# Optimization experiments

Hardware: AMD Instinct MI355X
Metric: run time of the kernel (lower is better)

## Reference

```python
import jax, jax.numpy as jnp
import numpy as np

B = 64            # batch of graphs
E = 8978          # edge-simplices per graph (nodes of the Hodge-1 graph)
E2 = E // 2       # after Graclus pair-pooling
K = 4             # Laguerre polynomial order
DEG = 16          # avg degree of the (edge-)adjacency
SLOPE = 0.33      # LeakyReLU negative slope
EPS = 1e-5        # BatchNorm eps


def _make_edges(rng, b, n, deg):
    # block-diagonal batched edge list: each graph only connects within itself
    offs = np.repeat(np.arange(b, dtype=np.int64) * n, n * deg)
    dst = np.tile(np.repeat(np.arange(n, dtype=np.int64), deg), b) + offs
    src = rng.integers(0, n, size=b * n * deg) + offs
    return np.stack([src, dst]).astype(np.int32)


def setup_inputs() -> dict:
    rng = np.random.default_rng(0)
    ks = jax.random.split(jax.random.key(0), 12)
    N1 = B * E
    ei1 = _make_edges(rng, B, E, DEG)
    ei2 = _make_edges(rng, B, E2, DEG)
    return {
        "x_s": jax.random.normal(ks[0], (N1, 1), jnp.float32),
        "edge_index_s": jnp.asarray(ei1),
        "edge_weight_s": jax.random.uniform(ks[1], (ei1.shape[1],), jnp.float32) * (2.0 / DEG),
        "edge_index_s1": jnp.asarray(ei2),
        "edge_weight_s1": jax.random.uniform(ks[2], (ei2.shape[1],), jnp.float32) * (2.0 / DEG),
        "W0": jax.random.normal(ks[3], (K, 1, 32), jnp.float32) * 0.3,
        "b0": jnp.zeros((32,), jnp.float32),
        "g0": jnp.ones((32,), jnp.float32),
        "be0": jnp.zeros((32,), jnp.float32),
        "W1": jax.random.normal(ks[4], (K, 32, 32), jnp.float32) * 0.1,
        "b1": jnp.zeros((32,), jnp.float32),
        "g1": jnp.ones((32,), jnp.float32),
        "be1": jnp.zeros((32,), jnp.float32),
        "W2": jax.random.normal(ks[5], (K, 32, 1), jnp.float32) * 0.1,
        "b2": jnp.zeros((1,), jnp.float32),
        "g2": jnp.ones((1,), jnp.float32),
        "be2": jnp.zeros((1,), jnp.float32),
        "lin1_W": jax.random.normal(ks[6], (E2, 256), jnp.float32) * 0.02,
        "lin1_b": jnp.zeros((256,), jnp.float32),
        "bn1_g": jnp.ones((256,), jnp.float32),
        "bn1_b": jnp.zeros((256,), jnp.float32),
        "lin2_W": jax.random.normal(ks[7], (256, 128), jnp.float32) * 0.06,
        "lin2_b": jnp.zeros((128,), jnp.float32),
        "bn2_g": jnp.ones((128,), jnp.float32),
        "bn2_b": jnp.zeros((128,), jnp.float32),
        "lin3_W": jax.random.normal(ks[8], (128, 1), jnp.float32) * 0.09,
        "lin3_b": jnp.zeros((1,), jnp.float32),
    }


def _laguerre_layer(x, src, dst, ew, W, b, gamma, beta, n):
    """HodgeLaguerreConv (K-order Laguerre recurrence over sparse L) + BatchNorm + LeakyReLU."""
    def matvec(v):  # (L v)[i] = sum_j w_ij v[j]
        return jax.ops.segment_sum(ew[:, None] * v[src], dst, num_segments=n)
    Tp = x                      # L_0(L) x = x
    out = Tp @ W[0]
    Tc = x - matvec(x)          # L_1(L) x = x - L x
    out = out + Tc @ W[1]
    for k in range(1, K - 1):   # L_{k+1} = ((2k+1-L) L_k - k L_{k-1}) / (k+1)
        Tn = ((2 * k + 1) * Tc - matvec(Tc) - k * Tp) / (k + 1)
        out = out + Tn @ W[k + 1]
        Tp, Tc = Tc, Tn
    out = out + b
    out = gamma * (out - out.mean(0)) * jax.lax.rsqrt(out.var(0) + EPS) + beta
    return jnp.where(out > 0, out, SLOPE * out)


def _bn(h, g, b):
    return g * (h - h.mean(0)) * jax.lax.rsqrt(h.var(0) + EPS) + b


def reference(x_s, edge_index_s, edge_weight_s, edge_index_s1, edge_weight_s1,
              W0, b0, g0, be0, W1, b1, g1, be1, W2, b2, g2, be2,
              lin1_W, lin1_b, bn1_g, bn1_b, lin2_W, lin2_b, bn2_g, bn2_b,
              lin3_W, lin3_b):
    N1, N2 = B * E, B * E2
    x = _laguerre_layer(x_s, edge_index_s[0], edge_index_s[1], edge_weight_s,
                        W0, b0, g0, be0, N1)
    # Graclus pooling: merge matched node pairs by max over features
    x = x.reshape(B, E2, 2, x.shape[-1]).max(axis=2).reshape(N2, -1)
    x = _laguerre_layer(x, edge_index_s1[0], edge_index_s1[1], edge_weight_s1,
                        W1, b1, g1, be1, N2)
    x = _laguerre_layer(x, edge_index_s1[0], edge_index_s1[1], edge_weight_s1,
                        W2, b2, g2, be2, N2)
    x = x.reshape(B, E2)        # last conv has 1 channel
    h = jax.nn.relu(_bn(x @ lin1_W + lin1_b, bn1_g, bn1_b))
    h = jax.nn.relu(_bn(h @ lin2_W + lin2_b, bn2_g, bn2_b))
    return h @ lin3_W + lin3_b  # [B, num_classes=1]
```

## Files before the change

### kernel.cpp

```cpp
#include <hip/hip_runtime.h>
#include <cstdint>

#define SLOPE 0.33f

static constexpr int B_   = 64;
static constexpr int E1_  = 8978;
static constexpr int E2_  = 4489;
static constexpr int N1_  = B_ * E1_;
static constexpr int N2_  = B_ * E2_;
static constexpr int DEG_ = 16;
static constexpr int QTR_ = 2245;
static constexpr int QTR2_ = 1123;
static constexpr int MVGRID = (N2_ * 32) / 256;
static constexpr int PROJ_GRID = (N2_ + 511) / 512;
static constexpr double EPS_ = 1e-5;

__device__ __forceinline__ float lrelu(float v) { return v > 0.f ? v : SLOPE * v; }
__device__ __forceinline__ float dot4(float4 a, float4 b) {
  return a.x * b.x + a.y * b.y + a.z * b.z + a.w * b.w;
}

__global__ __launch_bounds__(256) void k0_mv1(const float* __restrict__ x,
    const int* __restrict__ src, const float* __restrict__ ew, float* __restrict__ T1) {
  __shared__ float sx[E1_];
  int g = blockIdx.x >> 2, q = blockIdx.x & 3;
  int gbase = g * E1_;
  for (int j = threadIdx.x; j < E1_; j += 256) sx[j] = x[gbase + j];
  __syncthreads();
  int start = q * QTR_, end = min(start + QTR_, E1_);
  for (int i = start + (int)threadIdx.x; i < end; i += 256) {
    int node = gbase + i;
    const int4* s4 = (const int4*)(src + (size_t)node * DEG_);
    const float4* w4 = (const float4*)(ew + (size_t)node * DEG_);
    float acc = 0.f;
#pragma unroll
    for (int j = 0; j < 4; ++j) {
      int4 s = s4[j]; float4 w = w4[j];
      acc += w.x * sx[s.x - gbase] + w.y * sx[s.y - gbase]
           + w.z * sx[s.z - gbase] + w.w * sx[s.w - gbase];
    }
    T1[node] = sx[i] - acc;
  }
}

__global__ __launch_bounds__(256) void k0_mv2(const float* __restrict__ x,
    const int* __restrict__ src, const float* __restrict__ ew,
    const float* __restrict__ T1, float* __restrict__ T2) {
  __shared__ float sT[E1_];
  int g = blockIdx.x >> 2, q = blockIdx.x & 3;
  int gbase = g * E1_;
  for (int j = threadIdx.x; j < E1_; j += 256) sT[j] = T1[gbase + j];
  __syncthreads();
  int start = q * QTR_, end = min(start + QTR_, E1_);
  for (int i = start + (int)threadIdx.x; i < end; i += 256) {
    int node = gbase + i;
    const int4* s4 = (const int4*)(src + (size_t)node * DEG_);
    const float4* w4 = (const float4*)(ew + (size_t)node * DEG_);
    float acc = 0.f;
#pragma unroll
    for (int j = 0; j < 4; ++j) {
      int4 s = s4[j]; float4 w = w4[j];
      acc += w.x * sT[s.x - gbase] + w.y * sT[s.y - gbase]
           + w.z * sT[s.z - gbase] + w.w * sT[s.w - gbase];
    }
    T2[node] = (3.f * sT[i] - acc - x[node]) * 0.5f;
  }
}

__global__ __launch_bounds__(256) void k0_mv3(const float* __restrict__ x,
    const int* __restrict__ src, const float* __restrict__ ew,
    const float* __restrict__ T1, const float* __restrict__ T2,
    float* __restrict__ T3, double* mom) {
  __shared__ float sT[E1_];
  __shared__ double sred[4 * 14];
  int g = blockIdx.x >> 2, q = blockIdx.x & 3;
  int gbase = g * E1_;
  for (int j = threadIdx.x; j < E1_; j += 256) sT[j] = T2[gbase + j];
  __syncthreads();
  double m[14];
#pragma unroll
  for (int j = 0; j < 14; ++j) m[j] = 0.0;
  int start = q * QTR_, end = min(start + QTR_, E1_);
  for (int i = start + (int)threadIdx.x; i < end; i += 256) {
    int node = gbase + i;
    const int4* s4 = (const int4*)(src + (size_t)node * DEG_);
    const float4* w4 = (const float4*)(ew + (size_t)node * DEG_);
    float acc = 0.f;
#pragma unroll
    for (int j = 0; j < 4; ++j) {
      int4 s = s4[j]; float4 w = w4[j];
      acc += w.x * sT[s.x - gbase] + w.y * sT[s.y - gbase]
           + w.z * sT[s.z - gbase] + w.w * sT[s.w - gbase];
    }
    float t1 = T1[node];
    float t2 = sT[i];
    float t3 = (5.f * t2 - acc - 2.f * t1) * (1.f / 3.f);
    T3[node] = t3;
    double d0 = x[node], d1 = t1, d2 = t2, d3 = t3;
    m[0] += d0; m[1] += d1; m[2] += d2; m[3] += d3;
    m[4] += d0 * d0; m[5] += d0 * d1; m[6] += d0 * d2; m[7] += d0 * d3;
    m[8] += d1 * d1; m[9] += d1 * d2; m[10] += d1 * d3;
    m[11] += d2 * d2; m[12] += d2 * d3; m[13] += d3 * d3;
  }
  int lane = threadIdx.x & 63, wid = threadIdx.x >> 6;
#pragma unroll
  for (int j = 0; j < 14; ++j) {
    double v = m[j];
    for (int o = 32; o; o >>= 1) v += __shfl_down(v, o);
    if (lane == 0) sred[wid * 14 + j] = v;
  }
  __syncthreads();
  if (threadIdx.x < 14) {
    double s = sred[threadIdx.x] + sred[14 + threadIdx.x] + sred[28 + threadIdx.x] + sred[42 + threadIdx.x];
    atomicAdd(&mom[threadIdx.x], s);
  }
}

__global__ void k0_params(const double* __restrict__ mom, const float* __restrict__ W0,
    const float* __restrict__ g0, const float* __restrict__ be0,
    float* __restrict__ scale0, float* __restrict__ shiftE0) {
  int c = threadIdx.x;
  if (c >= 32) return;
  double inv = 1.0 / (double)N1_;
  double mm[4];
#pragma unroll
  for (int k = 0; k < 4; ++k) mm[k] = mom[k] * inv;
  double M[4][4];
  M[0][0] = mom[4] * inv;  M[0][1] = mom[5] * inv;  M[0][2] = mom[6] * inv;  M[0][3] = mom[7] * inv;
  M[1][1] = mom[8] * inv;  M[1][2] = mom[9] * inv;  M[1][3] = mom[10] * inv;
  M[2][2] = mom[11] * inv; M[2][3] = mom[12] * inv; M[3][3] = mom[13] * inv;
  M[1][0] = M[0][1]; M[2][0] = M[0][2]; M[3][0] = M[0][3];
  M[2][1] = M[1][2]; M[3][1] = M[1][3]; M[3][2] = M[2][3];
  double w[4];
#pragma unroll
  for (int k = 0; k < 4; ++k) w[k] = W0[k * 32 + c];
  double mean = 0.0;
#pragma unroll
  for (int k = 0; k < 4; ++k) mean += w[k] * mm[k];
  double e2 = 0.0;
#pragma unroll
  for (int k = 0; k < 4; ++k)
#pragma unroll
    for (int l = 0; l < 4; ++l) e2 += M[k][l] * w[k] * w[l];
  double var = e2 - mean * mean;
  double sc = (double)g0[c] / sqrt(var + EPS_);
  scale0[c] = (float)sc;
  shiftE0[c] = (float)((double)be0[c] - sc * mean);
}

__global__ __launch_bounds__(256) void k0_pool(const float* __restrict__ x,
    const float* __restrict__ T1, const float* __restrict__ T2, const float* __restrict__ T3,
    const float* __restrict__ W0, const float* __restrict__ scale0,
    const float* __restrict__ shiftE0, float* __restrict__ x1) {
  int gid = blockIdx.x * 256 + threadIdx.x;
  int grp = gid >> 5, c = gid & 31;
  if (grp >= N2_) return;
  int b = grp / E2_, j = grp - b * E2_;
  int ga = b * E1_ + 2 * j, gb = ga + 1;
  float w0 = W0[c], w1 = W0[32 + c], w2 = W0[64 + c], w3 = W0[96 + c];
  float da = x[ga] * w0 + T1[ga] * w1 + T2[ga] * w2 + T3[ga] * w3;
  float db = x[gb] * w0 + T1[gb] * w1 + T2[gb] * w2 + T3[gb] * w3;
  float sc = scale0[c], sh = shiftE0[c];
  float ya = lrelu(sc * da + sh), yb = lrelu(sc * db + sh);
  x1[grp * 32 + c] = fmaxf(ya, yb);
}

__global__ __launch_bounds__(256) void k1_projall(const float* __restrict__ X,
    const float* __restrict__ W1, float4* __restrict__ P4) {
  __shared__ float4 Wl[128 * 8];
  const float4 cfs[4] = { {0.f, 0.f, 0.f, -1.f / 6.f},
                          {0.f, 0.f, 0.5f, 1.5f},
                          {0.f, -1.f, -2.f, -3.f},
                          {1.f, 1.f, 1.f, 1.f} };
  for (int e = threadIdx.x; e < 1024; e += 256) {
    int o = e >> 3, qq = e & 7;
    int j = o >> 5, cp = o & 31;
    float4 cf = cfs[j];
    float4 w;
    {
      const float* wp = W1 + (4 * qq + 0) * 32 + cp;
      w.x = cf.x * wp[0] + cf.y * wp[1024] + cf.z * wp[2048] + cf.w * wp[3072];
    }
    {
      const float* wp = W1 + (4 * qq + 1) * 32 + cp;
      w.y = cf.x * wp[0] + cf.y * wp[1024] + cf.z * wp[2048] + cf.w * wp[3072];
    }
    {
      const float* wp = W1 + (4 * qq + 2) * 32 + cp;
      w.z = cf.x * wp[0] + cf.y * wp[1024] + cf.z * wp[2048] + cf.w * wp[3072];
    }
    {
      const float* wp = W1 + (4 * qq + 3) * 32 + cp;
      w.w = cf.x * wp[0] + cf.y * wp[1024] + cf.z * wp[2048] + cf.w * wp[3072];
    }
    Wl[e] = w;
  }
  __syncthreads();
  int rA = blockIdx.x * 512 + threadIdx.x;
  int rB = rA + 256;
  bool okA = rA < N2_, okB = rB < N2_;
  if (!okA) return;
  float4 xA[8], xB[8];
  {
    const float4* pa = (const float4*)(X + (size_t)rA * 32);
#pragma unroll
    for (int t = 0; t < 8; ++t) xA[t] = pa[t];
  }
  if (okB) {
    const float4* pb = (const float4*)(X + (size_t)rB * 32);
#pragma unroll
    for (int t = 0; t < 8; ++t) xB[t] = pb[t];
  } else {
#pragma unroll
    for (int t = 0; t < 8; ++t) xB[t] = {0.f, 0.f, 0.f, 0.f};
  }
  for (int oq = 0; oq < 32; ++oq) {
    float4 aA = {0.f, 0.f, 0.f, 0.f}, aB = {0.f, 0.f, 0.f, 0.f};
    const float4* wr = Wl + oq * 32;
#pragma unroll
    for (int qq = 0; qq < 8; ++qq) {
      float4 w0 = wr[0 * 8 + qq];
      float4 w1 = wr[1 * 8 + qq];
      float4 w2 = wr[2 * 8 + qq];
      float4 w3 = wr[3 * 8 + qq];
      float4 xa = xA[qq], xb = xB[qq];
      aA.x += dot4(xa, w0); aA.y += dot4(xa, w1); aA.z += dot4(xa, w2); aA.w += dot4(xa, w3);
      aB.x += dot4(xb, w0); aB.y += dot4(xb, w1); aB.z += dot4(xb, w2); aB.w += dot4(xb, w3);
    }
    P4[(size_t)oq * N2_ + rA] = aA;
    if (okB) P4[(size_t)oq * N2_ + rB] = aB;
  }
}

__global__ __launch_bounds__(1024) void k1_chain(const float4* __restrict__ P4,
    float4* __restrict__ O4, const int* __restrict__ src,
    const float* __restrict__ ew, double* st) {
  __shared__ float4 bA[E2_], bB[E2_];
  __shared__ float sacc[8];
  int v = (blockIdx.x & 7) * 64 + (blockIdx.x >> 3);
  int g = v >> 3, cg = v & 7;
  int gbase = g * E2_;
  int tid = threadIdx.x;
  if (tid < 8) sacc[tid] = 0.f;
  {
    const float4* sp = P4 + (size_t)cg * N2_ + gbase;
    for (int i = tid; i < E2_; i += 1024) bA[i] = sp[i];
  }
  float4* cur = bA;
  float4* nxt = bB;
  for (int s = 1; s <= 3; ++s) {
    __syncthreads();
    const float4* selfp = P4 + (size_t)(s * 8 + cg) * N2_ + gbase;
    for (int n = tid; n < E2_; n += 1024) {
      const int4* s4 = (const int4*)(src + (size_t)(gbase + n) * DEG_);
      const float4* w4 = (const float4*)(ew + (size_t)(gbase + n) * DEG_);
      float4 acc = selfp[n];
#pragma unroll
      for (int j = 0; j < 4; ++j) {
        int4 sx = s4[j]; float4 w = w4[j];
        float4 g0 = cur[sx.x - gbase];
        float4 g1 = cur[sx.y - gbase];
        float4 g2 = cur[sx.z - gbase];
        float4 g3 = cur[sx.w - gbase];
        acc.x += w.x * g0.x + w.y * g1.x + w.z * g2.x + w.w * g3.x;
        acc.y += w.x * g0.y + w.y * g1.y + w.z * g2.y + w.w * g3.y;
        acc.z += w.x * g0.z + w.y * g1.z + w.z * g2.z + w.w * g3.z;
        acc.w += w.x * g0.w + w.y * g1.w + w.z * g2.w + w.w * g3.w;
      }
      nxt[n] = acc;
    }
    float4* t = cur; cur = nxt; nxt = t;
  }
  __syncthreads();
  float4* op = O4 + (size_t)cg * N2_ + gbase;
  float4 s1 = {0.f, 0.f, 0.f, 0.f}, s2 = {0.f, 0.f, 0.f, 0.f};
  for (int n = tid; n < E2_; n += 1024) {
    float4 vv = cur[n];
    op[n] = vv;
    s1.x += vv.x; s1.y += vv.y; s1.z += vv.z; s1.w += vv.w;
    s2.x += vv.x * vv.x; s2.y += vv.y * vv.y; s2.z += vv.z * vv.z; s2.w += vv.w * vv.w;
  }
  for (int o = 32; o; o >>= 1) {
    s1.x += __shfl_down(s1.x, o); s1.y += __shfl_down(s1.y, o);
    s1.z += __shfl_down(s1.z, o); s1.w += __shfl_down(s1.w, o);
    s2.x += __shfl_down(s2.x, o); s2.y += __shfl_down(s2.y, o);
    s2.z += __shfl_down(s2.z, o); s2.w += __shfl_down(s2.w, o);
  }
  if ((tid & 63) == 0) {
    atomicAdd(&sacc[0], s1.x); atomicAdd(&sacc[1], s1.y);
    atomicAdd(&sacc[2], s1.z); atomicAdd(&sacc[3], s1.w);
    atomicAdd(&sacc[4], s2.x); atomicAdd(&sacc[5], s2.y);
    atomicAdd(&sacc[6], s2.z); atomicAdd(&sacc[7], s2.w);
  }
  __syncthreads();
  if (tid < 4) {
    int ch = cg * 4 + tid;
    atomicAdd(&st[ch], (double)sacc[tid]);
    atomicAdd(&st[32 + ch], (double)sacc[4 + tid]);
  }
}

__global__ void k1_params(const double* __restrict__ sum, const double* __restrict__ sq,
    const float* __restrict__ g1, const float* __restrict__ be1,
    float* __restrict__ scale1, float* __restrict__ shiftE1) {
  int c = threadIdx.x;
  if (c >= 32) return;
  double mean = sum[c] / (double)N2_;
  double var = sq[c] / (double)N2_ - mean * mean;
  double sc = (double)g1[c] / sqrt(var + EPS_);
  scale1[c] = (float)sc;
  shiftE1[c] = (float)((double)be1[c] - sc * mean);
}

__global__ __launch_bounds__(256) void k2_proj(const float* __restrict__ X,
    const float* __restrict__ W2, const float* __restrict__ scale1,
    const float* __restrict__ shiftE1,
    float* __restrict__ u0, float* __restrict__ u1,
    float* __restrict__ u2, float* __restrict__ u3) {
  __shared__ float qv[4][32];
  __shared__ float fsc[32], fsh[32];
  int tid = threadIdx.x;
  if (tid < 128) {
    int cp = tid & 31, j = tid >> 5;
    float w0 = W2[cp], w1 = W2[32 + cp], w2 = W2[64 + cp], w3 = W2[96 + cp];
    float q;
    if (j == 0)      q = w0 + w1 + w2 + w3;
    else if (j == 1) q = -w1 - 2.f * w2 - 3.f * w3;
    else if (j == 2) q = 0.5f * w2 + 1.5f * w3;
    else             q = -w3 * (1.f / 6.f);
    qv[j][cp] = q;
  }
  if (tid < 32) { fsc[tid] = scale1[tid]; fsh[tid] = shiftE1[tid]; }
  __syncthreads();
  int node = blockIdx.x * 256 + tid;
  if (node >= N2_) return;
  const float4* xf = (const float4*)X;
  float a0 = 0.f, a1 = 0.f, a2 = 0.f, a3 = 0.f;
#pragma unroll
  for (int t = 0; t < 8; ++t) {
    float4 v = xf[(size_t)t * N2_ + node];
    float f0 = lrelu(fsc[4 * t] * v.x + fsh[4 * t]);
    float f1 = lrelu(fsc[4 * t + 1] * v.y + fsh[4 * t + 1]);
    float f2_ = lrelu(fsc[4 * t + 2] * v.z + fsh[4 * t + 2]);
    float f3 = lrelu(fsc[4 * t + 3] * v.w + fsh[4 * t + 3]);
    a0 += f0 * qv[0][4 * t] + f1 * qv[0][4 * t + 1] + f2_ * qv[0][4 * t + 2] + f3 * qv[0][4 * t + 3];
    a1 += f0 * qv[1][4 * t] + f1 * qv[1][4 * t + 1] + f2_ * qv[1][4 * t + 2] + f3 * qv[1][4 * t + 3];
    a2 += f0 * qv[2][4 * t] + f1 * qv[2][4 * t + 1] + f2_ * qv[2][4 * t + 2] + f3 * qv[2][4 * t + 3];
    a3 += f0 * qv[3][4 * t] + f1 * qv[3][4 * t + 1] + f2_ * qv[3][4 * t + 2] + f3 * qv[3][4 * t + 3];
  }
  u0[node] = a0; u1[node] = a1; u2[node] = a2; u3[node] = a3;
}

__global__ __launch_bounds__(256) void k2_step(const float* __restrict__ z,
    const int* __restrict__ src, const float* __restrict__ ew,
    const float* __restrict__ u, float* __restrict__ zo,
    int do_stats, double* st2) {
  __shared__ float sz[E2_];
  __shared__ double sred[4][2];
  int g = blockIdx.x >> 2, q = blockIdx.x & 3;
  int gbase = g * E2_;
  for (int j = threadIdx.x; j < E2_; j += 256) sz[j] = z[gbase + j];
  __syncthreads();
  int start = q * QTR2_, end = min(start + QTR2_, E2_);
  double aS = 0.0, aQ = 0.0;
  for (int i = start + (int)threadIdx.x; i < end; i += 256) {
    int node = gbase + i;
    const int4* s4 = (const int4*)(src + (size_t)node * DEG_);
    const float4* w4 = (const float4*)(ew + (size_t)node * DEG_);
    float acc = 0.f;
#pragma unroll
    for (int j = 0; j < 4; ++j) {
      int4 s = s4[j]; float4 w = w4[j];
      acc += w.x * sz[s.x - gbase] + w.y * sz[s.y - gbase]
           + w.z * sz[s.z - gbase] + w.w * sz[s.w - gbase];
    }
    float val = u[node] + acc;
    zo[node] = val;
    if (do_stats) { aS += val; aQ += (double)val * (double)val; }
  }
  if (do_stats) {
    int lane = threadIdx.x & 63, wid = threadIdx.x >> 6;
    for (int o = 32; o; o >>= 1) { aS += __shfl_down(aS, o); aQ += __shfl_down(aQ, o); }
    if (lane == 0) { sred[wid][0] = aS; sred[wid][1] = aQ; }
    __syncthreads();
    if (threadIdx.x == 0) {
      double s = sred[0][0] + sred[1][0] + sred[2][0] + sred[3][0];
      double qq = sred[0][1] + sred[1][1] + sred[2][1] + sred[3][1];
      atomicAdd(&st2[0], s); atomicAdd(&st2[1], qq);
    }
  }
}

__global__ void k2_params(const double* __restrict__ st2, const float* __restrict__ g2,
    const float* __restrict__ be2, float* __restrict__ p ) {
  if (threadIdx.x != 0) return;
  double mean = st2[0] / (double)N2_;
  double var = st2[1] / (double)N2_ - mean * mean;
  double sc = (double)g2[0] / sqrt(var + EPS_);
  p[128] = (float)sc;
  p[129] = (float)((double)be2[0] - sc * mean);
}

__global__ __launch_bounds__(256) void k3_gemm1(const float* __restrict__ out2,
    const float* __restrict__ lin1W, const float* __restrict__ p, float* h1pre) {
  __shared__ float f2v[4][284];
  float sc = p[128], sh = p[129];
  int bs = blockIdx.x & 15, rs = blockIdx.x >> 4;
  int b0 = bs * 4;
  int r0 = rs * 281;
  int nr = min(281, E2_ - r0);
  int c = threadIdx.x;
#pragma unroll
  for (int b = 0; b < 4; ++b)
    for (int j = c; j < 284; j += 256)
      f2v[b][j] = (j < nr) ? lrelu(sc * out2[(b0 + b) * E2_ + r0 + j] + sh) : 0.f;
  __syncthreads();
  float acc0 = 0.f, acc1 = 0.f, acc2 = 0.f, acc3 = 0.f;
  int nr4 = nr & ~3;
  int j = 0;
  for (; j < nr4; j += 4) {
    const float* wp = lin1W + (size_t)(r0 + j) * 256 + c;
    float w0 = wp[0], w1 = wp[256], w2 = wp[512], w3 = wp[768];
    float4 f0 = *(const float4*)&f2v[0][j];
    float4 f1 = *(const float4*)&f2v[1][j];
    float4 f2_ = *(const float4*)&f2v[2][j];
    float4 f3 = *(const float4*)&f2v[3][j];
    acc0 += f0.x * w0 + f0.y * w1 + f0.z * w2 + f0.w * w3;
    acc1 += f1.x * w0 + f1.y * w1 + f1.z * w2 + f1.w * w3;
    acc2 += f2_.x * w0 + f2_.y * w1 + f2_.z * w2 + f2_.w * w3;
    acc3 += f3.x * w0 + f3.y * w1 + f3.z * w2 + f3.w * w3;
  }
  for (; j < nr; ++j) {
    float w = lin1W[(size_t)(r0 + j) * 256 + c];
    acc0 += f2v[0][j] * w;
    acc1 += f2v[1][j] * w;
    acc2 += f2v[2][j] * w;
    acc3 += f2v[3][j] * w;
  }
  atomicAdd(&h1pre[(b0 + 0) * 256 + c], acc0);
  atomicAdd(&h1pre[(b0 + 1) * 256 + c], acc1);
  atomicAdd(&h1pre[(b0 + 2) * 256 + c], acc2);
  atomicAdd(&h1pre[(b0 + 3) * 256 + c], acc3);
}

__global__ __launch_bounds__(256) void k4_bn1(const float* __restrict__ h1pre,
    const float* __restrict__ g, const float* __restrict__ be, float* __restrict__ h1) {
  int c = threadIdx.x;
  float vs[64];
  double s = 0.0, q = 0.0;
  for (int b = 0; b < 64; ++b) { float v = h1pre[b * 256 + c]; vs[b] = v; s += v; q += (double)v * v; }
  double mean = s / 64.0, var = q / 64.0 - mean * mean;
  double scd = (double)g[c] / sqrt(var + EPS_);
  double shd = (double)be[c] - scd * mean;
  for (int b = 0; b < 64; ++b) {
    float y = (float)(scd * vs[b] + shd);
    h1[b * 256 + c] = y > 0.f ? y : 0.f;
  }
}

__global__ __launch_bounds__(256) void k5_gemm2(const float* __restrict__ h1,
    const float* __restrict__ lin2W, float* __restrict__ h2pre) {
  __shared__ float sred[256];
  int c = blockIdx.x;
  int b = threadIdx.x & 63, q = threadIdx.x >> 6;
  float acc = 0.f;
  for (int r = q; r < 256; r += 4) acc += h1[b * 256 + r] * lin2W[r * 128 + c];
  sred[threadIdx.x] = acc;
  __syncthreads();
  if (threadIdx.x < 64)
    h2pre[threadIdx.x * 128 + c] = sred[threadIdx.x] + sred[64 + threadIdx.x]
                                 + sred[128 + threadIdx.x] + sred[192 + threadIdx.x];
}

__global__ __launch_bounds__(256) void k6_final(const float* __restrict__ h2pre,
    const float* __restrict__ g, const float* __restrict__ be,
    const float* __restrict__ W3, const float* __restrict__ b3, float* __restrict__ outp) {
  __shared__ float sh2[64 * 129];
  __shared__ float sred[256];
  int tid = threadIdx.x;
  if (tid < 128) {
    int c = tid;
    float vs[64];
    double s = 0.0, q = 0.0;
    for (int b = 0; b < 64; ++b) { float v = h2pre[b * 128 + c]; vs[b] = v; s += v; q += (double)v * v; }
    double mean = s / 64.0, var = q / 64.0 - mean * mean;
    double scd = (double)g[c] / sqrt(var + EPS_);
    double shd = (double)be[c] - scd * mean;
    for (int b = 0; b < 64; ++b) {
      float y = (float)(scd * vs[b] + shd);
      sh2[b * 129 + c] = y > 0.f ? y : 0.f;
    }
  }
  __syncthreads();
  int b = tid & 63, q = tid >> 6;
  float acc = 0.f;
  for (int r = q; r < 128; r += 4) acc += sh2[b * 129 + r] * W3[r];
  sred[tid] = acc;
  __syncthreads();
  if (tid < 64)
    outp[tid] = sred[tid] + sred[64 + tid] + sred[128 + tid] + sred[192 + tid] + b3[0];
}

extern "C" void kernel_launch(void* const* d_in, const int* in_sizes, int n_in,
                              void* d_out, int out_size, void* d_ws, size_t ws_size,
                              hipStream_t stream) {
  const float* x    = (const float*)d_in[0];
  const int*   ei1  = (const int*)d_in[1];
  const float* ew1  = (const float*)d_in[2];
  const int*   ei2  = (const int*)d_in[3];
  const float* ew2  = (const float*)d_in[4];
  const float* W0   = (const float*)d_in[5];
  const float* g0   = (const float*)d_in[7];
  const float* be0  = (const float*)d_in[8];
  const float* W1   = (const float*)d_in[9];
  const float* g1   = (const float*)d_in[11];
  const float* be1  = (const float*)d_in[12];
  const float* W2   = (const float*)d_in[13];
  const float* g2   = (const float*)d_in[15];
  const float* be2  = (const float*)d_in[16];
  const float* lin1W = (const float*)d_in[17];
  const float* bn1g = (const float*)d_in[19];
  const float* bn1b = (const float*)d_in[20];
  const float* lin2W = (const float*)d_in[21];
  const float* bn2g = (const float*)d_in[23];
  const float* bn2b = (const float*)d_in[24];
  const float* lin3W = (const float*)d_in[25];
  const float* lin3b = (const float*)d_in[26];

  char* ws = (char*)d_ws;
  double* stats  = (double*)ws;
  float*  params = (float*)(ws + 1024);
  float*  h1pre  = (float*)(ws + 4096);
  float*  h1     = (float*)(ws + 4096 + 65536);
  float*  h2pre  = (float*)(ws + 4096 + 131072);
  float*  Treg   = (float*)(ws + 262144);
  float* T1_0 = Treg;
  float* T2_0 = Treg + N1_;
  float* T3_0 = Treg + 2 * (size_t)N1_;
  float* u0   = Treg;
  float* u1   = Treg + (size_t)N2_;
  float* u2   = Treg + 2 * (size_t)N2_;
  float* u3   = Treg + 3 * (size_t)N2_;
  float* zA   = Treg + 4 * (size_t)N2_;
  float* out2 = Treg + 5 * (size_t)N2_;
  float*  big = (float*)(ws + 262144 + 3 * (size_t)N1_ * 4);
  float* bufA = big;
  float* Pbuf = big + 32 * (size_t)N2_;

  hipMemsetAsync(stats, 0, 80 * sizeof(double), stream);
  hipMemsetAsync(h1pre, 0, 65536, stream);

  k0_mv1<<<256, 256, 0, stream>>>(x, ei1, ew1, T1_0);
  k0_mv2<<<256, 256, 0, stream>>>(x, ei1, ew1, T1_0, T2_0);
  k0_mv3<<<256, 256, 0, stream>>>(x, ei1, ew1, T1_0, T2_0, T3_0, stats);
  k0_params<<<1, 32, 0, stream>>>(stats, W0, g0, be0, params, params + 32);
  k0_pool<<<MVGRID, 256, 0, stream>>>(x, T1_0, T2_0, T3_0, W0, params, params + 32, bufA);

  k1_projall<<<PROJ_GRID, 256, 0, stream>>>(bufA, W1, (float4*)Pbuf);
  k1_chain<<<512, 1024, 0, stream>>>((const float4*)Pbuf, (float4*)Pbuf, ei2, ew2, stats + 14);
  k1_params<<<1, 32, 0, stream>>>(stats + 14, stats + 46, g1, be1, params + 64, params + 96);

  k2_proj<<<(N2_ + 255) / 256, 256, 0, stream>>>(Pbuf, W2, params + 64, params + 96,
                                                 u0, u1, u2, u3);
  k2_step<<<256, 256, 0, stream>>>(u3, ei2, ew2, u2, zA, 0, nullptr);
  k2_step<<<256, 256, 0, stream>>>(zA, ei2, ew2, u1, u3, 0, nullptr);
  k2_step<<<256, 256, 0, stream>>>(u3, ei2, ew2, u0, out2, 1, stats + 78);
  k2_params<<<1, 64, 0, stream>>>(stats + 78, g2, be2, params);

  k3_gemm1<<<256, 256, 0, stream>>>(out2, lin1W, params, h1pre);
  k4_bn1<<<1, 256, 0, stream>>>(h1pre, bn1g, bn1b, h1);
  k5_gemm2<<<128, 256, 0, stream>>>(h1, lin2W, h2pre);
  k6_final<<<1, 256, 0, stream>>>(h2pre, bn2g, bn2b, lin3W, lin3b, (float*)d_out);
}
```

Before: 537.0 us.

## Split channel chain into float2 groups, enlarge blocks, and double gemm1 grid

The layer-1 chain kernel now processes 2 channels per block instead of 4. It launches 1024 blocks with half the shared memory, so more blocks can be resident at once, and the projection output layout changes to float2 planes to match. The sparse matvec kernels for layer 0 and layer 2 move from 256 to 1024 threads per block, with wider shared reductions. The first dense GEMM uses a smaller row slab per block and twice as many blocks. In exchange, each chain block must reload the graph's edge indices and weights twice as often, and the 1024-thread matvec blocks have only about 2245 nodes per block, so many threads go idle.

```diff
diff --git a/kernel.cpp b/kernel.cpp
--- a/kernel.cpp
+++ b/kernel.cpp
@@ -20,15 +20,15 @@
   return a.x * b.x + a.y * b.y + a.z * b.z + a.w * b.w;
 }
 
-__global__ __launch_bounds__(256) void k0_mv1(const float* __restrict__ x,
+__global__ __launch_bounds__(1024) void k0_mv1(const float* __restrict__ x,
     const int* __restrict__ src, const float* __restrict__ ew, float* __restrict__ T1) {
   __shared__ float sx[E1_];
   int g = blockIdx.x >> 2, q = blockIdx.x & 3;
   int gbase = g * E1_;
-  for (int j = threadIdx.x; j < E1_; j += 256) sx[j] = x[gbase + j];
+  for (int j = threadIdx.x; j < E1_; j += 1024) sx[j] = x[gbase + j];
   __syncthreads();
   int start = q * QTR_, end = min(start + QTR_, E1_);
-  for (int i = start + (int)threadIdx.x; i < end; i += 256) {
+  for (int i = start + (int)threadIdx.x; i < end; i += 1024) {
     int node = gbase + i;
     const int4* s4 = (const int4*)(src + (size_t)node * DEG_);
     const float4* w4 = (const float4*)(ew + (size_t)node * DEG_);
@@ -43,16 +43,16 @@
   }
 }
 
-__global__ __launch_bounds__(256) void k0_mv2(const float* __restrict__ x,
+__global__ __launch_bounds__(1024) void k0_mv2(const float* __restrict__ x,
     const int* __restrict__ src, const float* __restrict__ ew,
     const float* __restrict__ T1, float* __restrict__ T2) {
   __shared__ float sT[E1_];
   int g = blockIdx.x >> 2, q = blockIdx.x & 3;
   int gbase = g * E1_;
-  for (int j = threadIdx.x; j < E1_; j += 256) sT[j] = T1[gbase + j];
+  for (int j = threadIdx.x; j < E1_; j += 1024) sT[j] = T1[gbase + j];
   __syncthreads();
   int start = q * QTR_, end = min(start + QTR_, E1_);
-  for (int i = start + (int)threadIdx.x; i < end; i += 256) {
+  for (int i = start + (int)threadIdx.x; i < end; i += 1024) {
     int node = gbase + i;
     const int4* s4 = (const int4*)(src + (size_t)node * DEG_);
     const float4* w4 = (const float4*)(ew + (size_t)node * DEG_);
@@ -67,21 +67,21 @@
   }
 }
 
-__global__ __launch_bounds__(256) void k0_mv3(const float* __restrict__ x,
+__global__ __launch_bounds__(1024) void k0_mv3(const float* __restrict__ x,
     const int* __restrict__ src, const float* __restrict__ ew,
     const float* __restrict__ T1, const float* __restrict__ T2,
     float* __restrict__ T3, double* mom) {
   __shared__ float sT[E1_];
-  __shared__ double sred[4 * 14];
+  __shared__ double sred[16 * 14];
   int g = blockIdx.x >> 2, q = blockIdx.x & 3;
   int gbase = g * E1_;
-  for (int j = threadIdx.x; j < E1_; j += 256) sT[j] = T2[gbase + j];
+  for (int j = threadIdx.x; j < E1_; j += 1024) sT[j] = T2[gbase + j];
   __syncthreads();
   double m[14];
 #pragma unroll
   for (int j = 0; j < 14; ++j) m[j] = 0.0;
   int start = q * QTR_, end = min(start + QTR_, E1_);
-  for (int i = start + (int)threadIdx.x; i < end; i += 256) {
+  for (int i = start + (int)threadIdx.x; i < end; i += 1024) {
     int node = gbase + i;
     const int4* s4 = (const int4*)(src + (size_t)node * DEG_);
     const float4* w4 = (const float4*)(ew + (size_t)node * DEG_);
@@ -111,7 +111,9 @@
   }
   __syncthreads();
   if (threadIdx.x < 14) {
-    double s = sred[threadIdx.x] + sred[14 + threadIdx.x] + sred[28 + threadIdx.x] + sred[42 + threadIdx.x];
+    double s = 0.0;
+#pragma unroll
+    for (int w = 0; w < 16; ++w) s += sred[w * 14 + threadIdx.x];
     atomicAdd(&mom[threadIdx.x], s);
   }
 }
@@ -166,7 +168,7 @@
 }
 
 __global__ __launch_bounds__(256) void k1_projall(const float* __restrict__ X,
-    const float* __restrict__ W1, float4* __restrict__ P4) {
+    const float* __restrict__ W1, float2* __restrict__ P2b) {
   __shared__ float4 Wl[128 * 8];
   const float4 cfs[4] = { {0.f, 0.f, 0.f, -1.f / 6.f},
                           {0.f, 0.f, 0.5f, 1.5f},
@@ -227,76 +229,75 @@
       aA.x += dot4(xa, w0); aA.y += dot4(xa, w1); aA.z += dot4(xa, w2); aA.w += dot4(xa, w3);
       aB.x += dot4(xb, w0); aB.y += dot4(xb, w1); aB.z += dot4(xb, w2); aB.w += dot4(xb, w3);
     }
-    P4[(size_t)oq * N2_ + rA] = aA;
-    if (okB) P4[(size_t)oq * N2_ + rB] = aB;
-  }
-}
-
-__global__ __launch_bounds__(1024) void k1_chain(const float4* __restrict__ P4,
-    float4* __restrict__ O4, const int* __restrict__ src,
+    size_t base = (size_t)((oq >> 3) * 16 + (oq & 7) * 2) * N2_;
+    P2b[base + rA] = make_float2(aA.x, aA.y);
+    P2b[base + N2_ + rA] = make_float2(aA.z, aA.w);
+    if (okB) {
+      P2b[base + rB] = make_float2(aB.x, aB.y);
+      P2b[base + N2_ + rB] = make_float2(aB.z, aB.w);
+    }
+  }
+}
+
+__global__ __launch_bounds__(1024, 8) void k1_chain(const float2* __restrict__ P2b,
+    float2* __restrict__ O2, const int* __restrict__ src,
     const float* __restrict__ ew, double* st) {
-  __shared__ float4 bA[E2_], bB[E2_];
-  __shared__ float sacc[8];
-  int v = (blockIdx.x & 7) * 64 + (blockIdx.x >> 3);
-  int g = v >> 3, cg = v & 7;
+  __shared__ float2 bA[E2_], bB[E2_];
+  __shared__ float sacc[4];
+  int v = (blockIdx.x & 7) * 128 + (blockIdx.x >> 3);
+  int g = v >> 4, cg = v & 15;
   int gbase = g * E2_;
   int tid = threadIdx.x;
-  if (tid < 8) sacc[tid] = 0.f;
+  if (tid < 4) sacc[tid] = 0.f;
   {
-    const float4* sp = P4 + (size_t)cg * N2_ + gbase;
+    const float2* sp = P2b + (size_t)cg * N2_ + gbase;
     for (int i = tid; i < E2_; i += 1024) bA[i] = sp[i];
   }
-  float4* cur = bA;
-  float4* nxt = bB;
+  float2* cur = bA;
+  float2* nxt = bB;
   for (int s = 1; s <= 3; ++s) {
     __syncthreads();
-    const float4* selfp = P4 + (size_t)(s * 8 + cg) * N2_ + gbase;
+    const float2* selfp = P2b + (size_t)(s * 16 + cg) * N2_ + gbase;
     for (int n = tid; n < E2_; n += 1024) {
       const int4* s4 = (const int4*)(src + (size_t)(gbase + n) * DEG_);
       const float4* w4 = (const float4*)(ew + (size_t)(gbase + n) * DEG_);
-      float4 acc = selfp[n];
+      float2 acc = selfp[n];
 #pragma unroll
       for (int j = 0; j < 4; ++j) {
         int4 sx = s4[j]; float4 w = w4[j];
-        float4 g0 = cur[sx.x - gbase];
-        float4 g1 = cur[sx.y - gbase];
-        float4 g2 = cur[sx.z - gbase];
-        float4 g3 = cur[sx.w - gbase];
+        float2 g0 = cur[sx.x - gbase];
+        float2 g1 = cur[sx.y - gbase];
+        float2 g2 = cur[sx.z - gbase];
+        float2 g3 = cur[sx.w - gbase];
         acc.x += w.x * g0.x + w.y * g1.x + w.z * g2.x + w.w * g3.x;
         acc.y += w.x * g0.y + w.y * g1.y + w.z * g2.y + w.w * g3.y;
-        acc.z += w.x * g0.z + w.y * g1.z + w.z * g2.z + w.w * g3.z;
-        acc.w += w.x * g0.w + w.y * g1.w + w.z * g2.w + w.w * g3.w;
       }
       nxt[n] = acc;
     }
-    float4* t = cur; cur = nxt; nxt = t;
-  }
-  __syncthreads();
-  float4* op = O4 + (size_t)cg * N2_ + gbase;
-  float4 s1 = {0.f, 0.f, 0.f, 0.f}, s2 = {0.f, 0.f, 0.f, 0.f};
+    float2* t = cur; cur = nxt; nxt = t;
+  }
+  __syncthreads();
+  float2* op = O2 + (size_t)cg * N2_ + gbase;
+  float2 s1 = {0.f, 0.f}, s2 = {0.f, 0.f};
   for (int n = tid; n < E2_; n += 1024) {
-    float4 vv = cur[n];
+    float2 vv = cur[n];
     op[n] = vv;
-    s1.x += vv.x; s1.y += vv.y; s1.z += vv.z; s1.w += vv.w;
-    s2.x += vv.x * vv.x; s2.y += vv.y * vv.y; s2.z += vv.z * vv.z; s2.w += vv.w * vv.w;
+    s1.x += vv.x; s1.y += vv.y;
+    s2.x += vv.x * vv.x; s2.y += vv.y * vv.y;
   }
   for (int o = 32; o; o >>= 1) {
     s1.x += __shfl_down(s1.x, o); s1.y += __shfl_down(s1.y, o);
-    s1.z += __shfl_down(s1.z, o); s1.w += __shfl_down(s1.w, o);
     s2.x += __shfl_down(s2.x, o); s2.y += __shfl_down(s2.y, o);
-    s2.z += __shfl_down(s2.z, o); s2.w += __shfl_down(s2.w, o);
   }
   if ((tid & 63) == 0) {
     atomicAdd(&sacc[0], s1.x); atomicAdd(&sacc[1], s1.y);
-    atomicAdd(&sacc[2], s1.z); atomicAdd(&sacc[3], s1.w);
-    atomicAdd(&sacc[4], s2.x); atomicAdd(&sacc[5], s2.y);
-    atomicAdd(&sacc[6], s2.z); atomicAdd(&sacc[7], s2.w);
-  }
-  __syncthreads();
-  if (tid < 4) {
-    int ch = cg * 4 + tid;
+    atomicAdd(&sacc[2], s2.x); atomicAdd(&sacc[3], s2.y);
+  }
+  __syncthreads();
+  if (tid < 2) {
+    int ch = cg * 2 + tid;
     atomicAdd(&st[ch], (double)sacc[tid]);
-    atomicAdd(&st[32 + ch], (double)sacc[4 + tid]);
+    atomicAdd(&st[32 + ch], (double)sacc[2 + tid]);
   }
 }
 
@@ -334,36 +335,34 @@
   __syncthreads();
   int node = blockIdx.x * 256 + tid;
   if (node >= N2_) return;
-  const float4* xf = (const float4*)X;
+  const float2* xf = (const float2*)X;
   float a0 = 0.f, a1 = 0.f, a2 = 0.f, a3 = 0.f;
 #pragma unroll
-  for (int t = 0; t < 8; ++t) {
-    float4 v = xf[(size_t)t * N2_ + node];
-    float f0 = lrelu(fsc[4 * t] * v.x + fsh[4 * t]);
-    float f1 = lrelu(fsc[4 * t + 1] * v.y + fsh[4 * t + 1]);
-    float f2_ = lrelu(fsc[4 * t + 2] * v.z + fsh[4 * t + 2]);
-    float f3 = lrelu(fsc[4 * t + 3] * v.w + fsh[4 * t + 3]);
-    a0 += f0 * qv[0][4 * t] + f1 * qv[0][4 * t + 1] + f2_ * qv[0][4 * t + 2] + f3 * qv[0][4 * t + 3];
-    a1 += f0 * qv[1][4 * t] + f1 * qv[1][4 * t + 1] + f2_ * qv[1][4 * t + 2] + f3 * qv[1][4 * t + 3];
-    a2 += f0 * qv[2][4 * t] + f1 * qv[2][4 * t + 1] + f2_ * qv[2][4 * t + 2] + f3 * qv[2][4 * t + 3];
-    a3 += f0 * qv[3][4 * t] + f1 * qv[3][4 * t + 1] + f2_ * qv[3][4 * t + 2] + f3 * qv[3][4 * t + 3];
+  for (int t = 0; t < 16; ++t) {
+    float2 v = xf[(size_t)t * N2_ + node];
+    float f0 = lrelu(fsc[2 * t] * v.x + fsh[2 * t]);
+    float f1 = lrelu(fsc[2 * t + 1] * v.y + fsh[2 * t + 1]);
+    a0 += f0 * qv[0][2 * t] + f1 * qv[0][2 * t + 1];
+    a1 += f0 * qv[1][2 * t] + f1 * qv[1][2 * t + 1];
+    a2 += f0 * qv[2][2 * t] + f1 * qv[2][2 * t + 1];
+    a3 += f0 * qv[3][2 * t] + f1 * qv[3][2 * t + 1];
   }
   u0[node] = a0; u1[node] = a1; u2[node] = a2; u3[node] = a3;
 }
 
-__global__ __launch_bounds__(256) void k2_step(const float* __restrict__ z,
+__global__ __launch_bounds__(1024) void k2_step(const float* __restrict__ z,
     const int* __restrict__ src, const float* __restrict__ ew,
     const float* __restrict__ u, float* __restrict__ zo,
     int do_stats, double* st2) {
   __shared__ float sz[E2_];
-  __shared__ double sred[4][2];
+  __shared__ double sred[16][2];
   int g = blockIdx.x >> 2, q = blockIdx.x & 3;
   int gbase = g * E2_;
-  for (int j = threadIdx.x; j < E2_; j += 256) sz[j] = z[gbase + j];
+  for (int j = threadIdx.x; j < E2_; j += 1024) sz[j] = z[gbase + j];
   __syncthreads();
   int start = q * QTR2_, end = min(start + QTR2_, E2_);
   double aS = 0.0, aQ = 0.0;
-  for (int i = start + (int)threadIdx.x; i < end; i += 256) {
+  for (int i = start + (int)threadIdx.x; i < end; i += 1024) {
     int node = gbase + i;
     const int4* s4 = (const int4*)(src + (size_t)node * DEG_);
     const float4* w4 = (const float4*)(ew + (size_t)node * DEG_);
@@ -384,8 +383,9 @@
     if (lane == 0) { sred[wid][0] = aS; sred[wid][1] = aQ; }
     __syncthreads();
     if (threadIdx.x == 0) {
-      double s = sred[0][0] + sred[1][0] + sred[2][0] + sred[3][0];
-      double qq = sred[0][1] + sred[1][1] + sred[2][1] + sred[3][1];
+      double s = 0.0, qq = 0.0;
+#pragma unroll
+      for (int w = 0; w < 16; ++w) { s += sred[w][0]; qq += sred[w][1]; }
       atomicAdd(&st2[0], s); atomicAdd(&st2[1], qq);
     }
   }
@@ -403,16 +403,16 @@
 
 __global__ __launch_bounds__(256) void k3_gemm1(const float* __restrict__ out2,
     const float* __restrict__ lin1W, const float* __restrict__ p, float* h1pre) {
-  __shared__ float f2v[4][284];
+  __shared__ float f2v[4][144];
   float sc = p[128], sh = p[129];
   int bs = blockIdx.x & 15, rs = blockIdx.x >> 4;
   int b0 = bs * 4;
-  int r0 = rs * 281;
-  int nr = min(281, E2_ - r0);
+  int r0 = rs * 141;
+  int nr = min(141, E2_ - r0);
   int c = threadIdx.x;
 #pragma unroll
   for (int b = 0; b < 4; ++b)
-    for (int j = c; j < 284; j += 256)
+    for (int j = c; j < 144; j += 256)
       f2v[b][j] = (j < nr) ? lrelu(sc * out2[(b0 + b) * E2_ + r0 + j] + sh) : 0.f;
   __syncthreads();
   float acc0 = 0.f, acc1 = 0.f, acc2 = 0.f, acc3 = 0.f;
@@ -550,24 +550,24 @@
   hipMemsetAsync(stats, 0, 80 * sizeof(double), stream);
   hipMemsetAsync(h1pre, 0, 65536, stream);
 
-  k0_mv1<<<256, 256, 0, stream>>>(x, ei1, ew1, T1_0);
-  k0_mv2<<<256, 256, 0, stream>>>(x, ei1, ew1, T1_0, T2_0);
-  k0_mv3<<<256, 256, 0, stream>>>(x, ei1, ew1, T1_0, T2_0, T3_0, stats);
+  k0_mv1<<<256, 1024, 0, stream>>>(x, ei1, ew1, T1_0);
+  k0_mv2<<<256, 1024, 0, stream>>>(x, ei1, ew1, T1_0, T2_0);
+  k0_mv3<<<256, 1024, 0, stream>>>(x, ei1, ew1, T1_0, T2_0, T3_0, stats);
   k0_params<<<1, 32, 0, stream>>>(stats, W0, g0, be0, params, params + 32);
   k0_pool<<<MVGRID, 256, 0, stream>>>(x, T1_0, T2_0, T3_0, W0, params, params + 32, bufA);
 
-  k1_projall<<<PROJ_GRID, 256, 0, stream>>>(bufA, W1, (float4*)Pbuf);
-  k1_chain<<<512, 1024, 0, stream>>>((const float4*)Pbuf, (float4*)Pbuf, ei2, ew2, stats + 14);
+  k1_projall<<<PROJ_GRID, 256, 0, stream>>>(bufA, W1, (float2*)Pbuf);
+  k1_chain<<<1024, 1024, 0, stream>>>((const float2*)Pbuf, (float2*)Pbuf, ei2, ew2, stats + 14);
   k1_params<<<1, 32, 0, stream>>>(stats + 14, stats + 46, g1, be1, params + 64, params + 96);
 
   k2_proj<<<(N2_ + 255) / 256, 256, 0, stream>>>(Pbuf, W2, params + 64, params + 96,
                                                  u0, u1, u2, u3);
-  k2_step<<<256, 256, 0, stream>>>(u3, ei2, ew2, u2, zA, 0, nullptr);
-  k2_step<<<256, 256, 0, stream>>>(zA, ei2, ew2, u1, u3, 0, nullptr);
-  k2_step<<<256, 256, 0, stream>>>(u3, ei2, ew2, u0, out2, 1, stats + 78);
+  k2_step<<<256, 1024, 0, stream>>>(u3, ei2, ew2, u2, zA, 0, nullptr);
+  k2_step<<<256, 1024, 0, stream>>>(zA, ei2, ew2, u1, u3, 0, nullptr);
+  k2_step<<<256, 1024, 0, stream>>>(u3, ei2, ew2, u0, out2, 1, stats + 78);
   k2_params<<<1, 64, 0, stream>>>(stats + 78, g2, be2, params);
 
-  k3_gemm1<<<256, 256, 0, stream>>>(out2, lin1W, params, h1pre);
+  k3_gemm1<<<512, 256, 0, stream>>>(out2, lin1W, params, h1pre);
   k4_bn1<<<1, 256, 0, stream>>>(h1pre, bn1g, bn1b, h1);
   k5_gemm2<<<128, 256, 0, stream>>>(h1, lin2W, h2pre);
   k6_final<<<1, 256, 0, stream>>>(h2pre, bn2g, bn2b, lin3W, lin3b, (float*)d_out);
```

New measurement: 601.5 us. 1.12x slower.
